# Performance work log

Measured on AMD Instinct MI355X. Metric: run time of the kernel, lower is better.

Reference implementation:

```python
import jax, jax.numpy as jnp
import numpy as np

B, N, K, E = 4096, 64, 128, 512  # batch, n_cont_cols, max_num_buckets, embed_dim
EPS = 1e-8


def setup_inputs() -> dict:
    key = jax.random.key(0)
    kx, kw = jax.random.split(key)
    X = jax.random.uniform(kx, (B, N), dtype=jnp.float32)  # values in [0,1)
    # 129 sorted boundaries per column spanning [0,1] (same for every column)
    boundaries = jnp.tile(jnp.linspace(0.0, 1.0, K + 1, dtype=jnp.float32)[None, :], (N, 1))
    weight = jax.random.normal(kw, (N, K, E), dtype=jnp.float32) * 0.01  # init.normal_(std=0.01)
    bias = jnp.zeros((N, E), dtype=jnp.float32)  # init.zeros_
    return {"X": X, "boundaries": boundaries, "weight": weight, "bias": bias}


def reference(X, boundaries, weight, bias):
    # X: [B,N], boundaries: [N,K+1] sorted, weight: [N,K,E], bias: [N,E]
    Bn, Nc = X.shape
    Kb = weight.shape[1]
    # torch.bucketize(feat, bnd[1:-1], right=False) == searchsorted(side='left'); result in [0, K-1]
    inner = boundaries[:, 1:-1]  # [N, K-1]
    bidx = jax.vmap(lambda b, f: jnp.searchsorted(b, f, side='left'),
                    in_axes=(0, 1), out_axes=1)(inner, X)  # [B,N] int32
    cols = jnp.arange(Nc)[None, :]  # [1,N]
    start = boundaries[cols, bidx]        # [B,N]
    end = boundaries[cols, bidx + 1]      # [B,N]
    frac = (X - start) / (end - start + EPS)  # fractional position within bucket
    # greater_mask[b,n,k] = float(X[b,n] > boundaries[n,k]) for k in [0, K-1]
    greater = (X[:, :, None] > boundaries[None, :, :-1]).astype(X.dtype)  # [B,N,K]
    # scatter-assign frac at each sample's bucket index
    mask = jnp.where(jnp.arange(Kb)[None, None, :] == bidx[:, :, None],
                     frac[:, :, None], greater)  # [B,N,K]
    x = jnp.einsum('bnk,nke->bne', mask, weight) + bias[None]  # [B,N,E]
    x = jax.nn.relu(x)  # activation_fn='relu'
    # nn.Dropout is identity in eval mode
    return x
```

## Files before the change

### kernel.cpp

```cpp
#include <hip/hip_runtime.h>


#define BB 4096
#define NN 64
#define KK 128
#define EE 512
#define EPSF 1e-8f

__global__ void cumsum_kernel(const float* __restrict__ weight,
                              const float* __restrict__ bias,
                              float* __restrict__ C) {
    int n = blockIdx.x >> 1;
    int e = ((blockIdx.x & 1) << 8) + threadIdx.x;
    const float* w = weight + ((size_t)n * KK) * EE + e;
    float*       c = C + ((size_t)n * (KK + 1)) * EE + e;
    float run = bias[n * EE + e];
    c[0] = run;
#pragma unroll 8
    for (int k = 0; k < KK; ++k) {
        run += w[(size_t)k * EE];
        c[(size_t)(k + 1) * EE] = run;
    }
}

__global__ void idx_kernel(const float* __restrict__ X,
                           const float* __restrict__ boundaries,
                           int* __restrict__ bidx_out,
                           float* __restrict__ frac_out) {
    int i = blockIdx.x * blockDim.x + threadIdx.x;
    int n = i & (NN - 1);
    float x = X[i];
    const float* bnd = boundaries + n * (KK + 1);
    int lo = 0, hi = KK - 1;
    while (lo < hi) {
        int mid = (lo + hi) >> 1;
        if (bnd[1 + mid] < x) lo = mid + 1; else hi = mid;
    }
    float start = bnd[lo];
    float end   = bnd[lo + 1];
    bidx_out[i] = lo;
    frac_out[i] = (x - start) / (end - start + EPSF);
}

__global__ void gather_kernel(const float* __restrict__ C,
                              const int* __restrict__ bidx,
                              const float* __restrict__ frac,
                              float* __restrict__ out) {
    int base = blockIdx.x << 2;
    int e = threadIdx.x << 1;
#pragma unroll
    for (int it = 0; it < 4; ++it) {
        int t = base + it;
        int n = t >> 12;
        int b = t & (BB - 1);
        int i = b * NN + n;
        int bi = __ldg(&bidx[i]);
        float f = __ldg(&frac[i]);
        const float2* c0 =
            (const float2*)(C + (((size_t)n * (KK + 1) + bi) * EE) + e);
        float2 lo = c0[0];
        float2 hi = c0[EE / 2];
        float2 r;
        r.x = fmaf(f, hi.x - lo.x, lo.x);
        r.y = fmaf(f, hi.y - lo.y, lo.y);
        r.x = fmaxf(r.x, 0.f);
        r.y = fmaxf(r.y, 0.f);
        *(float2*)(out + ((size_t)b * NN + n) * EE + e) = r;
    }
}

extern "C" void kernel_launch(void* const* d_in, const int* in_sizes, int n_in,
                              void* d_out, int out_size, void* d_ws, size_t ws_size,
                              hipStream_t stream) {
    const float* X          = (const float*)d_in[0];
    const float* boundaries = (const float*)d_in[1];
    const float* weight     = (const float*)d_in[2];
    const float* bias       = (const float*)d_in[3];
    float* out = (float*)d_out;

    float* C = (float*)d_ws;
    size_t Csz = (size_t)NN * (KK + 1) * EE;
    int*   bidx = (int*)(C + Csz);
    float* frac = (float*)(bidx + (size_t)BB * NN);

    cumsum_kernel<<<NN * (EE / 256), 256, 0, stream>>>(weight, bias, C);
    idx_kernel<<<(BB * NN) / 256, 256, 0, stream>>>(X, boundaries, bidx, frac);
    gather_kernel<<<(BB * NN) / 4, 256, 0, stream>>>(C, bidx, frac, out);
}
```

Before: 594.1 us.

## Parallelize cumsum across K segments, pack index/frac, widen gather stores

```diff
diff --git a/kernel.cpp b/kernel.cpp
--- a/kernel.cpp
+++ b/kernel.cpp
@@ -7,27 +7,46 @@
 #define EE 512
 #define EPSF 1e-8f
 
-__global__ void cumsum_kernel(const float* __restrict__ weight,
-                              const float* __restrict__ bias,
-                              float* __restrict__ C) {
-    int n = blockIdx.x >> 1;
-    int e = ((blockIdx.x & 1) << 8) + threadIdx.x;
-    const float* w = weight + ((size_t)n * KK) * EE + e;
-    float*       c = C + ((size_t)n * (KK + 1)) * EE + e;
-    float run = bias[n * EE + e];
-    c[0] = run;
-#pragma unroll 8
-    for (int k = 0; k < KK; ++k) {
-        run += w[(size_t)k * EE];
-        c[(size_t)(k + 1) * EE] = run;
+typedef float f32x4 __attribute__((ext_vector_type(4)));
+
+__global__ __launch_bounds__(256) void cumsum_kernel(
+        const float* __restrict__ weight,
+        const float* __restrict__ bias,
+        float* __restrict__ C) {
+    int n   = blockIdx.x >> 3;
+    int e0  = (blockIdx.x & 7) << 6;
+    int ec  = threadIdx.x & 63;
+    int seg = threadIdx.x >> 6;
+    int e   = e0 + ec;
+
+    const float* w = weight + ((size_t)(n * KK + seg * 32)) * EE + e;
+    float r[32];
+    float run = 0.f;
+#pragma unroll
+    for (int kk = 0; kk < 32; ++kk) {
+        run += __builtin_nontemporal_load(&w[(size_t)kk * EE]);
+        r[kk] = run;
     }
+
+    __shared__ float part[4][64];
+    part[seg][ec] = run;
+    __syncthreads();
+
+    float off = bias[n * EE + e];
+    for (int s = 0; s < seg; ++s) off += part[s][ec];
+
+    if (seg == 0) C[((size_t)n * (KK + 1)) * EE + e] = off;
+    float* c = C + ((size_t)(n * (KK + 1) + seg * 32 + 1)) * EE + e;
+#pragma unroll
+    for (int kk = 0; kk < 32; ++kk)
+        c[(size_t)kk * EE] = off + r[kk];
 }
 
-__global__ void idx_kernel(const float* __restrict__ X,
-                           const float* __restrict__ boundaries,
-                           int* __restrict__ bidx_out,
-                           float* __restrict__ frac_out) {
-    int i = blockIdx.x * blockDim.x + threadIdx.x;
+__global__ __launch_bounds__(256) void idx_kernel(
+        const float* __restrict__ X,
+        const float* __restrict__ boundaries,
+        int2* __restrict__ pack) {
+    int i = blockIdx.x * 256 + threadIdx.x;
     int n = i & (NN - 1);
     float x = X[i];
     const float* bnd = boundaries + n * (KK + 1);
@@ -36,36 +55,45 @@
         int mid = (lo + hi) >> 1;
         if (bnd[1 + mid] < x) lo = mid + 1; else hi = mid;
     }
-    float start = bnd[lo];
-    float end   = bnd[lo + 1];
-    bidx_out[i] = lo;
-    frac_out[i] = (x - start) / (end - start + EPSF);
+    float s = bnd[lo];
+    float en = bnd[lo + 1];
+    int2 p;
+    p.x = lo;
+    p.y = __float_as_int((x - s) / (en - s + EPSF));
+    pack[i] = p;
 }
 
-__global__ void gather_kernel(const float* __restrict__ C,
-                              const int* __restrict__ bidx,
-                              const float* __restrict__ frac,
-                              float* __restrict__ out) {
-    int base = blockIdx.x << 2;
-    int e = threadIdx.x << 1;
+__global__ __launch_bounds__(256) void gather_kernel(
+        const float* __restrict__ C,
+        const int2* __restrict__ pack,
+        float* __restrict__ out) {
+    int base = blockIdx.x << 3;
+    int g    = threadIdx.x >> 7;
+    int e    = (threadIdx.x & 127) << 2;
+
+    int n = base >> 12;
+    const float* Cn = C + ((size_t)n * (KK + 1)) * EE;
+
 #pragma unroll
     for (int it = 0; it < 4; ++it) {
-        int t = base + it;
-        int n = t >> 12;
+        int t = base + (g << 2) + it;
         int b = t & (BB - 1);
         int i = b * NN + n;
-        int bi = __ldg(&bidx[i]);
-        float f = __ldg(&frac[i]);
-        const float2* c0 =
-            (const float2*)(C + (((size_t)n * (KK + 1) + bi) * EE) + e);
-        float2 lo = c0[0];
-        float2 hi = c0[EE / 2];
-        float2 r;
-        r.x = fmaf(f, hi.x - lo.x, lo.x);
-        r.y = fmaf(f, hi.y - lo.y, lo.y);
-        r.x = fmaxf(r.x, 0.f);
-        r.y = fmaxf(r.y, 0.f);
-        *(float2*)(out + ((size_t)b * NN + n) * EE + e) = r;
+        int2 p = pack[i];
+        int   bi = p.x;
+        float f  = __int_as_float(p.y);
+
+        const f32x4* c0 = (const f32x4*)(Cn + (size_t)bi * EE + e);
+        f32x4 lo = c0[0];
+        f32x4 hi = c0[EE / 4];
+        f32x4 r;
+        r.x = fmaxf(fmaf(f, hi.x - lo.x, lo.x), 0.f);
+        r.y = fmaxf(fmaf(f, hi.y - lo.y, lo.y), 0.f);
+        r.z = fmaxf(fmaf(f, hi.z - lo.z, lo.z), 0.f);
+        r.w = fmaxf(fmaf(f, hi.w - lo.w, lo.w), 0.f);
+
+        f32x4* dst = (f32x4*)(out + ((size_t)b * NN + n) * EE + e);
+        __builtin_nontemporal_store(r, dst);
     }
 }
 
@@ -80,10 +108,9 @@
 
     float* C = (float*)d_ws;
     size_t Csz = (size_t)NN * (KK + 1) * EE;
-    int*   bidx = (int*)(C + Csz);
-    float* frac = (float*)(bidx + (size_t)BB * NN);
+    int2* pack = (int2*)(C + Csz);
 
-    cumsum_kernel<<<NN * (EE / 256), 256, 0, stream>>>(weight, bias, C);
-    idx_kernel<<<(BB * NN) / 256, 256, 0, stream>>>(X, boundaries, bidx, frac);
-    gather_kernel<<<(BB * NN) / 4, 256, 0, stream>>>(C, bidx, frac, out);
+    cumsum_kernel<<<NN * (EE / 64), 256, 0, stream>>>(weight, bias, C);
+    idx_kernel<<<(BB * NN) / 256, 256, 0, stream>>>(X, boundaries, pack);
+    gather_kernel<<<(BB * NN) / 8, 256, 0, stream>>>(C, pack, out);
 }
```

New measurement: 554.4 us. 1.07x faster.
